# Performance work log

Hardware: AMD Instinct MI355X
Metric: run time of the kernel (lower is better)

The kernel has to match this reference:

```python
import jax, jax.numpy as jnp
import numpy as np

PATCH_LEN = 16


def _forward(x, W_proj, b_proj, W_router, b_router, W_experts, b_experts, W_head, b_head):
    # x: (B, L, C); Model drops first 2 channels
    seq_len = x.shape[1]
    xs = x[:, :, 2:]                                   # (B, L, N)
    B, L, N = xs.shape
    # CI=True: 'b l n -> (b n) l 1' (track as (BN, L) since trailing dim is 1)
    ci = jnp.transpose(xs, (0, 2, 1)).reshape(B * N, L)
    # RevIN-style instance norm (means detached in torch)
    means = jax.lax.stop_gradient(jnp.mean(ci, axis=1, keepdims=True))
    xc = ci - means
    stdev = jnp.sqrt(jnp.var(xc, axis=1, keepdims=True) + 1e-5)  # unbiased=False
    xc = xc / stdev
    # non-overlapping patching: unfold(1, pl, pl)
    p = L // PATCH_LEN
    patches = xc[:, : p * PATCH_LEN].reshape(B * N, p, PATCH_LEN)
    xp = patches @ W_proj.T + b_proj                   # (BN, p, d)
    gates = jax.nn.softmax(xp @ W_router.T + b_router, axis=-1)  # (BN, p, E)
    # soft-routed mixture of linear experts: sum_e gate_e * (xp @ W_e^T + b_e)
    eo = jnp.einsum('tpd,ehd->tpeh', xp, W_experts) + b_experts  # (BN, p, E, d)
    combined = jnp.einsum('tpeh,tpe->tph', eo, gates)            # (BN, p, d)
    d = combined.shape[-1]
    flat = combined.reshape(B * N, p * d)              # '(b n) p d -> b (p d) n', n=1
    if p * d < seq_len:
        flat = jnp.pad(flat, ((0, 0), (0, seq_len - p * d)))
    else:
        flat = flat[:, :seq_len]
    flat = flat * stdev + means                        # de-normalize (BN, L)
    # '(b n) l 1 -> b l n' then 'b l n -> b n l' == reshape to (B, N, L)
    temporal = flat.reshape(B, N, seq_len)
    out = temporal @ W_head.T + b_head                 # linear_head: (B, N, pred)
    out = jnp.transpose(out, (0, 2, 1))[:, :, :1]      # 'b n d -> b d n', keep var 0
    return out


def setup_inputs() -> dict:
    key = jax.random.key(0)
    ks = jax.random.split(key, 12)
    B, L, C = 32, 1024, 34
    d, E, pl, pred = 256, 8, PATCH_LEN, 96
    return {
        'x': jax.random.normal(ks[0], (B, L, C), dtype=jnp.float32),
        'x_mark_enc': jax.random.normal(ks[1], (B, L, 4), dtype=jnp.float32),
        'x_dec': jax.random.normal(ks[2], (B, pred, C), dtype=jnp.float32),
        'x_mark_dec': jax.random.normal(ks[3], (B, pred, 4), dtype=jnp.float32),
        'W_proj': jax.random.normal(ks[4], (d, pl), dtype=jnp.float32) * 0.1,
        'b_proj': jax.random.normal(ks[5], (d,), dtype=jnp.float32) * 0.02,
        'W_router': jax.random.normal(ks[6], (E, d), dtype=jnp.float32) * 0.05,
        'b_router': jax.random.normal(ks[7], (E,), dtype=jnp.float32) * 0.02,
        'W_experts': jax.random.normal(ks[8], (E, d, d), dtype=jnp.float32) * 0.05,
        'b_experts': jax.random.normal(ks[9], (E, d), dtype=jnp.float32) * 0.02,
        'W_head': jax.random.normal(ks[10], (pred, L), dtype=jnp.float32) * 0.03,
        'b_head': jax.random.normal(ks[11], (pred,), dtype=jnp.float32) * 0.02,
    }


def reference(x, x_mark_enc, x_dec, x_mark_dec, W_proj, b_proj, W_router, b_router,
              W_experts, b_experts, W_head, b_head):
    # x_mark_enc, x_dec, x_mark_dec are accepted but unused by Model.forward
    return _forward(x, W_proj, b_proj, W_router, b_router,
                    W_experts, b_experts, W_head, b_head)
```

## Files before the change

### kernel.cpp

```cpp
#include <hip/hip_runtime.h>
#include <math.h>


#define NB 32
#define LSEQ 1024
#define CCH 34
#define NP 4
#define DMODEL 256
#define NEXP 8
#define PRED 96
#define NPART (2 * NEXP)

#define WT_FLOATS    (NEXP * DMODEL * DMODEL)
#define XP_FLOATS    (NB * NP * DMODEL)
#define GATES_FLOATS (NB * NP * NEXP)
#define STATS_FLOATS (NB * 2)

__global__ __launch_bounds__(256) void k_stats(
    const float* __restrict__ x,
    const float* __restrict__ W_proj, const float* __restrict__ b_proj,
    const float* __restrict__ W_router, const float* __restrict__ b_router,
    const float* __restrict__ W_experts, float* __restrict__ Wt,
    float* __restrict__ xp_ws, float* __restrict__ gates_ws,
    float* __restrict__ stats_ws)
{
    const int bid = blockIdx.x;
    const int tid = threadIdx.x;
    const int b = bid;

    __shared__ float tile[64][33];
    __shared__ float xn[LSEQ];
    __shared__ float xp_s[NP * DMODEL];
    __shared__ float red[8];
    __shared__ float lg[32];
    __shared__ float mean_s, rstd_s;

    float v[4];
    if (b < NB) {
        #pragma unroll
        for (int i = 0; i < 4; ++i)
            v[i] = x[(size_t)(b * LSEQ + tid + 256 * i) * CCH + 2];
    }

    {
        const int e  = bid >> 5;
        const int h0 = ((bid >> 3) & 3) << 6;
        const int d0 = (bid & 7) << 5;
        const float* src = W_experts + ((size_t)e << 16);
        float*       dst = Wt        + ((size_t)e << 16);
        const int dx = tid & 31, hy = tid >> 5;
        const int hx = tid & 63, dy = tid >> 6;
        #pragma unroll
        for (int i = 0; i < 8; ++i) {
            const int hh = hy + 8 * i;
            tile[hh][dx] = src[(size_t)(h0 + hh) * DMODEL + d0 + dx];
        }
        __syncthreads();
        #pragma unroll
        for (int i = 0; i < 8; ++i) {
            const int dd = dy + 4 * i;
            dst[(size_t)(d0 + dd) * DMODEL + h0 + hx] = tile[hx][dd];
        }
    }

    if (b >= NB) return;

    float s = 0.f, sq = 0.f;
    #pragma unroll
    for (int i = 0; i < 4; ++i) { s += v[i]; sq += v[i] * v[i]; }
    #pragma unroll
    for (int off = 32; off > 0; off >>= 1) {
        s  += __shfl_down(s,  off);
        sq += __shfl_down(sq, off);
    }
    const int wave = tid >> 6;
    if ((tid & 63) == 0) { red[wave * 2] = s; red[wave * 2 + 1] = sq; }
    __syncthreads();
    if (tid == 0) {
        const float S = red[0] + red[2] + red[4] + red[6];
        const float Q = red[1] + red[3] + red[5] + red[7];
        const float mean = S * (1.0f / LSEQ);
        const float var  = Q * (1.0f / LSEQ) - mean * mean;
        const float stdv = sqrtf(var + 1e-5f);
        mean_s = mean;
        rstd_s = 1.0f / stdv;
        stats_ws[b * 2]     = mean;
        stats_ws[b * 2 + 1] = stdv;
    }
    __syncthreads();
    const float mean = mean_s, rstd = rstd_s;
    #pragma unroll
    for (int i = 0; i < 4; ++i)
        xn[tid + 256 * i] = (v[i] - mean) * rstd;
    __syncthreads();

    {
        const int h = tid;
        float wrow[16];
        #pragma unroll
        for (int j = 0; j < 16; ++j) wrow[j] = W_proj[h * 16 + j];
        const float bp = b_proj[h];
        #pragma unroll
        for (int p = 0; p < NP; ++p) {
            float acc = bp;
            #pragma unroll
            for (int j = 0; j < 16; ++j) acc += xn[p * 16 + j] * wrow[j];
            xp_s[p * DMODEL + h] = acc;
            xp_ws[((size_t)b * NP + p) * DMODEL + h] = acc;
        }
    }
    __syncthreads();

    if (tid < 32) {
        const int p = tid >> 3, e = tid & 7;
        float acc = b_router[e];
        const float* wr = W_router + e * DMODEL;
        const float* xp = xp_s + p * DMODEL;
        #pragma unroll 8
        for (int h = 0; h < DMODEL; ++h) acc += xp[h] * wr[h];
        lg[tid] = acc;
    }
    __syncthreads();

    if (tid < NP) {
        const int p = tid;
        float m = -1e30f;
        #pragma unroll
        for (int e = 0; e < NEXP; ++e) m = fmaxf(m, lg[p * 8 + e]);
        float ex[NEXP];
        float sum = 0.f;
        #pragma unroll
        for (int e = 0; e < NEXP; ++e) { ex[e] = expf(lg[p * 8 + e] - m); sum += ex[e]; }
        const float inv = 1.0f / sum;
        #pragma unroll
        for (int e = 0; e < NEXP; ++e)
            gates_ws[((size_t)b * NP + p) * NEXP + e] = ex[e] * inv;
    }
}

__global__ __launch_bounds__(256, 4) void k_expert(
    const float* __restrict__ Wt, const float* __restrict__ b_experts,
    const float* __restrict__ xp_ws, const float* __restrict__ gates_ws,
    float* __restrict__ flat_part)
{
    const int bid = blockIdx.x;
    const int bg2 = bid >> 6;
    const int r   = bid & 63;
    const int hq  = r >> 4;
    const int dh  = (r >> 3) & 1;
    const int e   = r & 7;
    const int b0  = bg2 * 2;
    const int tid = threadIdx.x;
    const int p   = tid >> 6;
    const int hl  = tid & 63;
    const int h   = (hq << 6) + hl;
    const int d0  = dh << 7;

    __shared__ float xp_s[2 * NP * DMODEL];
    __shared__ float g_s[2 * NP * NEXP];

    {
        const float4* src = (const float4*)(xp_ws + ((size_t)b0 << 10));
        float4* dst = (float4*)xp_s;
        dst[tid]       = src[tid];
        dst[tid + 256] = src[tid + 256];
    }
    if (tid < 64) g_s[tid] = gates_ws[(size_t)b0 * (NP * NEXP) + tid];
    __syncthreads();

    const float* wt  = Wt + ((size_t)e << 16) + ((size_t)d0 << 8) + h;
    const float4* xpA = (const float4*)(xp_s + (p << 8) + d0);
    const float4* xpB = (const float4*)(xp_s + ((4 + p) << 8) + d0);

    float a0 = 0.f, a1 = 0.f;
    #pragma unroll 8
    for (int q = 0; q < 32; ++q) {
        const float w0 = wt[(size_t)(4 * q + 0) << 8];
        const float w1 = wt[(size_t)(4 * q + 1) << 8];
        const float w2 = wt[(size_t)(4 * q + 2) << 8];
        const float w3 = wt[(size_t)(4 * q + 3) << 8];
        const float4 xA = xpA[q];
        const float4 xB = xpB[q];
        a0 += w0 * xA.x + w1 * xA.y + w2 * xA.z + w3 * xA.w;
        a1 += w0 * xB.x + w1 * xB.y + w2 * xB.z + w3 * xB.w;
    }

    const float g0 = g_s[(p << 3) + e];
    const float g1 = g_s[32 + (p << 3) + e];
    const float bias = (dh == 0) ? b_experts[(e << 8) + h] : 0.f;
    const int part = (e << 1) | dh;
    flat_part[(((size_t)part * NB + b0)     << 10) + (p << 8) + h] = g0 * (a0 + bias);
    flat_part[(((size_t)part * NB + b0 + 1) << 10) + (p << 8) + h] = g1 * (a1 + bias);
}

__global__ __launch_bounds__(256) void k_head(
    const float* __restrict__ flat_part, const float* __restrict__ stats_ws,
    const float* __restrict__ W_head, const float* __restrict__ b_head,
    float* __restrict__ out)
{
    const int b   = blockIdx.x >> 3;
    const int kq  = blockIdx.x & 7;
    const int tid = threadIdx.x;
    __shared__ float4 f4s[DMODEL];

    const float mean = stats_ws[b * 2];
    const float stdv = stats_ws[b * 2 + 1];

    {
        float4 acc = make_float4(0.f, 0.f, 0.f, 0.f);
        #pragma unroll
        for (int i = 0; i < NPART; ++i) {
            const float4 t = ((const float4*)(flat_part + (((size_t)i * NB + b) << 10)))[tid];
            acc.x += t.x; acc.y += t.y; acc.z += t.z; acc.w += t.w;
        }
        acc.x = acc.x * stdv + mean;
        acc.y = acc.y * stdv + mean;
        acc.z = acc.z * stdv + mean;
        acc.w = acc.w * stdv + mean;
        f4s[tid] = acc;
    }
    __syncthreads();

    const int lane = tid & 63;
    const int w    = tid >> 6;
    float4 fr[4];
    #pragma unroll
    for (int c = 0; c < 4; ++c) fr[c] = f4s[lane + 64 * c];

    #pragma unroll
    for (int i = 0; i < 3; ++i) {
        const int k = kq * 12 + w + 4 * i;
        const float4* wr = (const float4*)(W_head + (size_t)k * LSEQ);
        float a = 0.f;
        #pragma unroll
        for (int c = 0; c < 4; ++c) {
            const float4 t = wr[lane + 64 * c];
            a += t.x * fr[c].x + t.y * fr[c].y + t.z * fr[c].z + t.w * fr[c].w;
        }
        #pragma unroll
        for (int off = 32; off > 0; off >>= 1)
            a += __shfl_xor(a, off);
        if (lane == 0)
            out[(size_t)b * PRED + k] = b_head[k] + a;
    }
}

extern "C" void kernel_launch(void* const* d_in, const int* in_sizes, int n_in,
                              void* d_out, int out_size, void* d_ws, size_t ws_size,
                              hipStream_t stream)
{
    const float* x         = (const float*)d_in[0];
    const float* W_proj    = (const float*)d_in[4];
    const float* b_proj    = (const float*)d_in[5];
    const float* W_router  = (const float*)d_in[6];
    const float* b_router  = (const float*)d_in[7];
    const float* W_experts = (const float*)d_in[8];
    const float* b_experts = (const float*)d_in[9];
    const float* W_head    = (const float*)d_in[10];
    const float* b_head    = (const float*)d_in[11];
    float* out = (float*)d_out;
    float* ws  = (float*)d_ws;

    float* Wt        = ws;
    float* xp_ws     = ws + WT_FLOATS;
    float* gates_ws  = xp_ws + XP_FLOATS;
    float* stats_ws  = gates_ws + GATES_FLOATS;
    float* flat_part = stats_ws + STATS_FLOATS;

    k_stats<<<256, 256, 0, stream>>>(x, W_proj, b_proj, W_router, b_router,
                                     W_experts, Wt, xp_ws, gates_ws, stats_ws);
    k_expert<<<1024, 256, 0, stream>>>(Wt, b_experts, xp_ws, gates_ws, flat_part);
    k_head<<<256, 256, 0, stream>>>(flat_part, stats_ws, W_head, b_head, out);
}
```

Measured before the change: 100.7 us.

## Fuse stats, router and expert kernels into one per-batch-expert kernel

Merges the normalization/projection/router kernel and the expert matmul kernel into a single launch with one block per (batch, expert) pair. Each block transposes its expert weights through shared memory in 64-column chunks, loading the next chunk into registers while computing on the current one. This removes the global Wt transpose buffer, the xp and gates workspace round-trips, and one kernel launch. The router dot product also changes from 32 serial threads to all 256 threads with shuffle reductions. In exchange, each block recomputes the per-batch stats, projection and router (eight times redundant per batch) and reads a full 256 KB expert matrix.

```diff
diff --git a/kernel.cpp b/kernel.cpp
--- a/kernel.cpp
+++ b/kernel.cpp
@@ -9,90 +9,76 @@
 #define DMODEL 256
 #define NEXP 8
 #define PRED 96
-#define NPART (2 * NEXP)
-
-#define WT_FLOATS    (NEXP * DMODEL * DMODEL)
-#define XP_FLOATS    (NB * NP * DMODEL)
-#define GATES_FLOATS (NB * NP * NEXP)
+#define DT 64
+#define NPART NEXP
+
 #define STATS_FLOATS (NB * 2)
 
-__global__ __launch_bounds__(256) void k_stats(
+__global__ __launch_bounds__(256) void k_fused(
     const float* __restrict__ x,
     const float* __restrict__ W_proj, const float* __restrict__ b_proj,
     const float* __restrict__ W_router, const float* __restrict__ b_router,
-    const float* __restrict__ W_experts, float* __restrict__ Wt,
-    float* __restrict__ xp_ws, float* __restrict__ gates_ws,
-    float* __restrict__ stats_ws)
+    const float* __restrict__ W_experts, const float* __restrict__ b_experts,
+    float* __restrict__ flat_part, float* __restrict__ stats_ws)
 {
     const int bid = blockIdx.x;
+    const int e   = bid & 7;
+    const int b   = bid >> 3;
     const int tid = threadIdx.x;
-    const int b = bid;
-
-    __shared__ float tile[64][33];
+
+    __shared__ float wtT[DT][DMODEL + 1];
     __shared__ float xn[LSEQ];
     __shared__ float xp_s[NP * DMODEL];
     __shared__ float red[8];
     __shared__ float lg[32];
+    __shared__ float g_s[NP];
     __shared__ float mean_s, rstd_s;
 
     float v[4];
-    if (b < NB) {
+    #pragma unroll
+    for (int i = 0; i < 4; ++i)
+        v[i] = x[(size_t)(b * LSEQ + tid + 256 * i) * CCH + 2];
+
+    const int c4 = tid & 15;
+    const int hb = tid >> 4;
+    const float* wsrc = W_experts + ((size_t)e << 16);
+    float4 wreg[16];
+    #pragma unroll
+    for (int i = 0; i < 16; ++i)
+        wreg[i] = *(const float4*)(wsrc + (size_t)(hb + 16 * i) * DMODEL + 4 * c4);
+
+    {
+        float s = 0.f, sq = 0.f;
+        #pragma unroll
+        for (int i = 0; i < 4; ++i) { s += v[i]; sq += v[i] * v[i]; }
+        #pragma unroll
+        for (int off = 32; off > 0; off >>= 1) {
+            s  += __shfl_down(s,  off);
+            sq += __shfl_down(sq, off);
+        }
+        const int wave = tid >> 6;
+        if ((tid & 63) == 0) { red[wave * 2] = s; red[wave * 2 + 1] = sq; }
+        __syncthreads();
+        if (tid == 0) {
+            const float S = red[0] + red[2] + red[4] + red[6];
+            const float Q = red[1] + red[3] + red[5] + red[7];
+            const float mean = S * (1.0f / LSEQ);
+            const float var  = Q * (1.0f / LSEQ) - mean * mean;
+            const float stdv = sqrtf(var + 1e-5f);
+            mean_s = mean;
+            rstd_s = 1.0f / stdv;
+            if (e == 0) {
+                stats_ws[b * 2]     = mean;
+                stats_ws[b * 2 + 1] = stdv;
+            }
+        }
+        __syncthreads();
+        const float mean = mean_s, rstd = rstd_s;
         #pragma unroll
         for (int i = 0; i < 4; ++i)
-            v[i] = x[(size_t)(b * LSEQ + tid + 256 * i) * CCH + 2];
-    }
-
-    {
-        const int e  = bid >> 5;
-        const int h0 = ((bid >> 3) & 3) << 6;
-        const int d0 = (bid & 7) << 5;
-        const float* src = W_experts + ((size_t)e << 16);
-        float*       dst = Wt        + ((size_t)e << 16);
-        const int dx = tid & 31, hy = tid >> 5;
-        const int hx = tid & 63, dy = tid >> 6;
-        #pragma unroll
-        for (int i = 0; i < 8; ++i) {
-            const int hh = hy + 8 * i;
-            tile[hh][dx] = src[(size_t)(h0 + hh) * DMODEL + d0 + dx];
-        }
-        __syncthreads();
-        #pragma unroll
-        for (int i = 0; i < 8; ++i) {
-            const int dd = dy + 4 * i;
-            dst[(size_t)(d0 + dd) * DMODEL + h0 + hx] = tile[hx][dd];
-        }
-    }
-
-    if (b >= NB) return;
-
-    float s = 0.f, sq = 0.f;
-    #pragma unroll
-    for (int i = 0; i < 4; ++i) { s += v[i]; sq += v[i] * v[i]; }
-    #pragma unroll
-    for (int off = 32; off > 0; off >>= 1) {
-        s  += __shfl_down(s,  off);
-        sq += __shfl_down(sq, off);
-    }
-    const int wave = tid >> 6;
-    if ((tid & 63) == 0) { red[wave * 2] = s; red[wave * 2 + 1] = sq; }
-    __syncthreads();
-    if (tid == 0) {
-        const float S = red[0] + red[2] + red[4] + red[6];
-        const float Q = red[1] + red[3] + red[5] + red[7];
-        const float mean = S * (1.0f / LSEQ);
-        const float var  = Q * (1.0f / LSEQ) - mean * mean;
-        const float stdv = sqrtf(var + 1e-5f);
-        mean_s = mean;
-        rstd_s = 1.0f / stdv;
-        stats_ws[b * 2]     = mean;
-        stats_ws[b * 2 + 1] = stdv;
-    }
-    __syncthreads();
-    const float mean = mean_s, rstd = rstd_s;
-    #pragma unroll
-    for (int i = 0; i < 4; ++i)
-        xn[tid + 256 * i] = (v[i] - mean) * rstd;
-    __syncthreads();
+            xn[tid + 256 * i] = (v[i] - mean) * rstd;
+        __syncthreads();
+    }
 
     {
         const int h = tid;
@@ -106,19 +92,25 @@
             #pragma unroll
             for (int j = 0; j < 16; ++j) acc += xn[p * 16 + j] * wrow[j];
             xp_s[p * DMODEL + h] = acc;
-            xp_ws[((size_t)b * NP + p) * DMODEL + h] = acc;
         }
     }
     __syncthreads();
 
-    if (tid < 32) {
-        const int p = tid >> 3, e = tid & 7;
-        float acc = b_router[e];
-        const float* wr = W_router + e * DMODEL;
-        const float* xp = xp_s + p * DMODEL;
+    {
+        const int pe = tid >> 3;
+        const int sl = tid & 7;
+        const int p  = pe >> 3;
+        const int er = pe & 7;
+        float acc = 0.f;
         #pragma unroll 8
-        for (int h = 0; h < DMODEL; ++h) acc += xp[h] * wr[h];
-        lg[tid] = acc;
+        for (int j = 0; j < 32; ++j) {
+            const int hh = sl + 8 * j;
+            acc += xp_s[p * DMODEL + hh] * W_router[er * DMODEL + hh];
+        }
+        acc += __shfl_xor(acc, 4);
+        acc += __shfl_xor(acc, 2);
+        acc += __shfl_xor(acc, 1);
+        if (sl == 0) lg[pe] = acc + b_router[er];
     }
     __syncthreads();
 
@@ -126,71 +118,49 @@
         const int p = tid;
         float m = -1e30f;
         #pragma unroll
-        for (int e = 0; e < NEXP; ++e) m = fmaxf(m, lg[p * 8 + e]);
+        for (int k = 0; k < NEXP; ++k) m = fmaxf(m, lg[p * 8 + k]);
         float ex[NEXP];
         float sum = 0.f;
         #pragma unroll
-        for (int e = 0; e < NEXP; ++e) { ex[e] = expf(lg[p * 8 + e] - m); sum += ex[e]; }
-        const float inv = 1.0f / sum;
-        #pragma unroll
-        for (int e = 0; e < NEXP; ++e)
-            gates_ws[((size_t)b * NP + p) * NEXP + e] = ex[e] * inv;
-    }
-}
-
-__global__ __launch_bounds__(256, 4) void k_expert(
-    const float* __restrict__ Wt, const float* __restrict__ b_experts,
-    const float* __restrict__ xp_ws, const float* __restrict__ gates_ws,
-    float* __restrict__ flat_part)
-{
-    const int bid = blockIdx.x;
-    const int bg2 = bid >> 6;
-    const int r   = bid & 63;
-    const int hq  = r >> 4;
-    const int dh  = (r >> 3) & 1;
-    const int e   = r & 7;
-    const int b0  = bg2 * 2;
-    const int tid = threadIdx.x;
-    const int p   = tid >> 6;
-    const int hl  = tid & 63;
-    const int h   = (hq << 6) + hl;
-    const int d0  = dh << 7;
-
-    __shared__ float xp_s[2 * NP * DMODEL];
-    __shared__ float g_s[2 * NP * NEXP];
-
-    {
-        const float4* src = (const float4*)(xp_ws + ((size_t)b0 << 10));
-        float4* dst = (float4*)xp_s;
-        dst[tid]       = src[tid];
-        dst[tid + 256] = src[tid + 256];
-    }
-    if (tid < 64) g_s[tid] = gates_ws[(size_t)b0 * (NP * NEXP) + tid];
-    __syncthreads();
-
-    const float* wt  = Wt + ((size_t)e << 16) + ((size_t)d0 << 8) + h;
-    const float4* xpA = (const float4*)(xp_s + (p << 8) + d0);
-    const float4* xpB = (const float4*)(xp_s + ((4 + p) << 8) + d0);
-
-    float a0 = 0.f, a1 = 0.f;
-    #pragma unroll 8
-    for (int q = 0; q < 32; ++q) {
-        const float w0 = wt[(size_t)(4 * q + 0) << 8];
-        const float w1 = wt[(size_t)(4 * q + 1) << 8];
-        const float w2 = wt[(size_t)(4 * q + 2) << 8];
-        const float w3 = wt[(size_t)(4 * q + 3) << 8];
-        const float4 xA = xpA[q];
-        const float4 xB = xpB[q];
-        a0 += w0 * xA.x + w1 * xA.y + w2 * xA.z + w3 * xA.w;
-        a1 += w0 * xB.x + w1 * xB.y + w2 * xB.z + w3 * xB.w;
-    }
-
-    const float g0 = g_s[(p << 3) + e];
-    const float g1 = g_s[32 + (p << 3) + e];
-    const float bias = (dh == 0) ? b_experts[(e << 8) + h] : 0.f;
-    const int part = (e << 1) | dh;
-    flat_part[(((size_t)part * NB + b0)     << 10) + (p << 8) + h] = g0 * (a0 + bias);
-    flat_part[(((size_t)part * NB + b0 + 1) << 10) + (p << 8) + h] = g1 * (a1 + bias);
+        for (int k = 0; k < NEXP; ++k) { ex[k] = expf(lg[p * 8 + k] - m); sum += ex[k]; }
+        g_s[p] = ex[e] / sum;
+    }
+
+    float acc0 = 0.f, acc1 = 0.f, acc2 = 0.f, acc3 = 0.f;
+    for (int t = 0; t < 4; ++t) {
+        __syncthreads();
+        #pragma unroll
+        for (int i = 0; i < 16; ++i) {
+            const int h = hb + 16 * i;
+            wtT[4 * c4 + 0][h] = wreg[i].x;
+            wtT[4 * c4 + 1][h] = wreg[i].y;
+            wtT[4 * c4 + 2][h] = wreg[i].z;
+            wtT[4 * c4 + 3][h] = wreg[i].w;
+        }
+        __syncthreads();
+        if (t < 3) {
+            #pragma unroll
+            for (int i = 0; i < 16; ++i)
+                wreg[i] = *(const float4*)(wsrc + (size_t)(hb + 16 * i) * DMODEL
+                                           + (t + 1) * DT + 4 * c4);
+        }
+        const float* xpp = xp_s + t * DT;
+        #pragma unroll 8
+        for (int c = 0; c < DT; ++c) {
+            const float wv = wtT[c][tid];
+            acc0 += xpp[c]       * wv;
+            acc1 += xpp[256 + c] * wv;
+            acc2 += xpp[512 + c] * wv;
+            acc3 += xpp[768 + c] * wv;
+        }
+    }
+
+    const float bias = b_experts[(e << 8) + tid];
+    const size_t base = ((size_t)(e * NB + b) << 10) + tid;
+    flat_part[base]         = g_s[0] * (acc0 + bias);
+    flat_part[base + 256]   = g_s[1] * (acc1 + bias);
+    flat_part[base + 512]   = g_s[2] * (acc2 + bias);
+    flat_part[base + 768]   = g_s[3] * (acc3 + bias);
 }
 
 __global__ __launch_bounds__(256) void k_head(
@@ -261,14 +231,10 @@
     float* out = (float*)d_out;
     float* ws  = (float*)d_ws;
 
-    float* Wt        = ws;
-    float* xp_ws     = ws + WT_FLOATS;
-    float* gates_ws  = xp_ws + XP_FLOATS;
-    float* stats_ws  = gates_ws + GATES_FLOATS;
-    float* flat_part = stats_ws + STATS_FLOATS;
-
-    k_stats<<<256, 256, 0, stream>>>(x, W_proj, b_proj, W_router, b_router,
-                                     W_experts, Wt, xp_ws, gates_ws, stats_ws);
-    k_expert<<<1024, 256, 0, stream>>>(Wt, b_experts, xp_ws, gates_ws, flat_part);
+    float* stats_ws  = ws;
+    float* flat_part = ws + STATS_FLOATS;
+
+    k_fused<<<256, 256, 0, stream>>>(x, W_proj, b_proj, W_router, b_router,
+                                     W_experts, b_experts, flat_part, stats_ws);
     k_head<<<256, 256, 0, stream>>>(flat_part, stats_ws, W_head, b_head, out);
 }
```

New measurement: 98.83 us. Within noise of the previous version (-1.9%).
